# Kernel tuning notes

Measured on AMD Instinct MI355X. Metric: run time of the kernel, lower is better.

## Reference

```python
import jax, jax.numpy as jnp
import numpy as np

D_MODEL = 2048
NUM_HEADS = 16
HEAD_DIM = D_MODEL // NUM_HEADS  # 128


def setup_inputs() -> dict:
    key = jax.random.key(0)
    ks = jax.random.split(key, 9)
    s = 0.02
    x = jax.random.normal(ks[0], (2, 2048, D_MODEL), dtype=jnp.float32)
    Wq = jax.random.normal(ks[1], (D_MODEL, D_MODEL), dtype=jnp.float32) * s
    bq = jnp.zeros((D_MODEL,), dtype=jnp.float32)
    Wk = jax.random.normal(ks[2], (D_MODEL, HEAD_DIM), dtype=jnp.float32) * s
    bk = jnp.zeros((HEAD_DIM,), dtype=jnp.float32)
    Wv = jax.random.normal(ks[3], (D_MODEL, HEAD_DIM), dtype=jnp.float32) * s
    bv = jnp.zeros((HEAD_DIM,), dtype=jnp.float32)
    Wo = jax.random.normal(ks[4], (D_MODEL, D_MODEL), dtype=jnp.float32) * s
    bo = jnp.zeros((D_MODEL,), dtype=jnp.float32)
    return {"x": x, "Wq": Wq, "bq": bq, "Wk": Wk, "bk": bk,
            "Wv": Wv, "bv": bv, "Wo": Wo, "bo": bo}


def reference(x, Wq, bq, Wk, bk, Wv, bv, Wo, bo):
    B, S, _ = x.shape
    # projections
    q = (x @ Wq + bq).reshape(B, S, NUM_HEADS, HEAD_DIM)  # [B,S,H,d]
    k = x @ Wk + bk  # [B,S,d] shared across heads (MQA)
    v = x @ Wv + bv  # [B,S,d]
    scale = 1.0 / jnp.sqrt(jnp.float32(HEAD_DIM))
    # QK^T with shared K: [B,H,Sq,Sk]
    scores = jnp.einsum('bqhd,bkd->bhqk', q, k) * scale
    attn = jax.nn.softmax(scores, axis=-1)
    # AV with shared V: [B,H,Sq,d]
    out = jnp.einsum('bhqk,bkd->bqhd', attn, v).reshape(B, S, D_MODEL)
    return out @ Wo + bo
```

## Files before the change

kernel.cpp:

```cpp
#include <hip/hip_runtime.h>


typedef __attribute__((ext_vector_type(8))) short short8;
typedef __attribute__((ext_vector_type(4))) float f32x4;
typedef __attribute__((ext_vector_type(4))) unsigned int uint4v;

__device__ __forceinline__ unsigned short f2bf(float f) {
  unsigned int u = __float_as_uint(f);
  u += 0x7FFF + ((u >> 16) & 1);
  return (unsigned short)(u >> 16);
}

__device__ __forceinline__ unsigned int pk2(float a, float b) {
  return (unsigned int)f2bf(a) | ((unsigned int)f2bf(b) << 16);
}

__device__ __forceinline__ void gll16(const void* g, void* lds) {
  __builtin_amdgcn_global_load_lds(
      (const __attribute__((address_space(1))) unsigned int*)g,
      (__attribute__((address_space(3))) unsigned int*)lds, 16, 0, 0);
}

__global__ __launch_bounds__(256) void cvtk(const float* __restrict__ in,
                                            unsigned short* __restrict__ out, int n4) {
  int i = blockIdx.x * blockDim.x + threadIdx.x;
  int stride = gridDim.x * blockDim.x;
  for (; i < n4; i += stride) {
    float4 v = reinterpret_cast<const float4*>(in)[i];
    ushort4 o;
    o.x = f2bf(v.x); o.y = f2bf(v.y); o.z = f2bf(v.z); o.w = f2bf(v.w);
    reinterpret_cast<ushort4*>(out)[i] = o;
  }
}

__global__ __launch_bounds__(256) void tcvt2(const float* __restrict__ W0, const float* __restrict__ W1,
                                             unsigned short* __restrict__ D0, unsigned short* __restrict__ D1,
                                             int K, int N) {
  const float* W = blockIdx.z ? W1 : W0;
  unsigned short* Wt = blockIdx.z ? D1 : D0;
  __shared__ float tile[32][33];
  int n0 = blockIdx.x * 32, k0 = blockIdx.y * 32;
  int tx = threadIdx.x, ty = threadIdx.y;
  #pragma unroll
  for (int i = 0; i < 32; i += 8)
    tile[ty + i][tx] = W[(size_t)(k0 + ty + i) * N + n0 + tx];
  __syncthreads();
  #pragma unroll
  for (int i = 0; i < 32; i += 8)
    Wt[(size_t)(n0 + ty + i) * K + k0 + tx] = f2bf(tile[tx][ty + i]);
}

template <int MODE>
__global__ __launch_bounds__(256)
void gemm_nt(const unsigned short* __restrict__ A, const unsigned short* __restrict__ Bt,
             const float* __restrict__ b0, const float* __restrict__ b1,
             const float* __restrict__ b2,
             void* __restrict__ C, unsigned short* __restrict__ C2,
             unsigned short* __restrict__ C3, int M, int N, int K, float cmul) {
  __shared__ unsigned short lA[128 * 64];
  __shared__ unsigned short lB[128 * 64];
  const int t = threadIdx.x;
  const int lane = t & 63;
  const int w = t >> 6;
  const int wr = w >> 1, wc = w & 1;
  const int r15 = lane & 15, g4 = lane >> 4;
  const int tileM = blockIdx.y * 128;
  const int tileN = blockIdx.x * 128;

  f32x4 acc[4][4];
  #pragma unroll
  for (int i = 0; i < 4; i++)
    #pragma unroll
    for (int j = 0; j < 4; j++) acc[i][j] = (f32x4){0.f, 0.f, 0.f, 0.f};

  const int nkt = K >> 6;
  for (int kt = 0; kt < nkt; ++kt) {
    const int k0 = kt * 64;
    #pragma unroll
    for (int i = 0; i < 4; ++i) {
      int flat = i * 256 + t;
      int row = flat >> 3, gc = flat & 7;
      unsigned lb = (unsigned)(i * 256 + w * 64) * 16;
      gll16(A  + (size_t)(tileM + row) * K + k0 + gc * 8, (char*)lA + lb);
      gll16(Bt + (size_t)(tileN + row) * K + k0 + gc * 8, (char*)lB + lb);
    }
    __syncthreads();
    #pragma unroll
    for (int kk = 0; kk < 2; ++kk) {
      short8 af[4], bf[4];
      #pragma unroll
      for (int mt = 0; mt < 4; ++mt)
        af[mt] = *reinterpret_cast<const short8*>(&lA[(wr * 64 + mt * 16 + r15) * 64 + kk * 32 + g4 * 8]);
      #pragma unroll
      for (int nt = 0; nt < 4; ++nt)
        bf[nt] = *reinterpret_cast<const short8*>(&lB[(wc * 64 + nt * 16 + r15) * 64 + kk * 32 + g4 * 8]);
      #pragma unroll
      for (int mt = 0; mt < 4; ++mt)
        #pragma unroll
        for (int nt = 0; nt < 4; ++nt)
          acc[mt][nt] = __builtin_amdgcn_mfma_f32_16x16x32_bf16(af[mt], bf[nt], acc[mt][nt], 0, 0, 0);
    }
    __syncthreads();
  }

  #pragma unroll
  for (int mt = 0; mt < 4; ++mt) {
    #pragma unroll
    for (int nt = 0; nt < 4; ++nt) {
      int col = tileN + wc * 64 + nt * 16 + r15;
      #pragma unroll
      for (int r = 0; r < 4; ++r) {
        int row = tileM + wr * 64 + mt * 16 + g4 * 4 + r;
        float v = acc[mt][nt][r];
        if (MODE == 1) {
          ((float*)C)[(size_t)row * N + col] = v + b0[col];
        } else {
          if (col < 2048) {
            ((unsigned short*)C)[(size_t)row * 2048 + col] = f2bf((v + b0[col]) * cmul);
          } else if (col < 2176) {
            int dd = col - 2048;
            C2[(size_t)row * 128 + dd] = f2bf(v + b1[dd]);
          } else {
            int dd = col - 2176;
            int bb = row >> 11, s = row & 2047;
            C3[((size_t)bb * 128 + dd) * 2048 + s] = f2bf(v + b2[dd]);
          }
        }
      }
    }
  }
}

__global__ __launch_bounds__(256)
void flash_mqa(const unsigned short* __restrict__ qb, const unsigned short* __restrict__ kb,
               const unsigned short* __restrict__ vt, unsigned short* __restrict__ ob) {
  __shared__ unsigned short lK[2][64 * 128];
  __shared__ unsigned short lV[2][128 * 64];
  __shared__ unsigned short lP[4][16 * 64];

  const int t = threadIdx.x;
  const int lane = t & 63;
  const int w = t >> 6;
  const int r15 = lane & 15, g4 = lane >> 4;
  const int qt = blockIdx.x, h = blockIdx.y, b = blockIdx.z;
  const int q0 = qt * 64 + w * 16;

  short8 qf[4];
  const size_t qrow = (size_t)(b * 2048 + q0 + r15);
  #pragma unroll
  for (int kk = 0; kk < 4; ++kk)
    qf[kk] = *reinterpret_cast<const short8*>(&qb[qrow * 2048 + h * 128 + kk * 32 + g4 * 8]);

  f32x4 oacc[8];
  #pragma unroll
  for (int i = 0; i < 8; i++) oacc[i] = (f32x4){0.f, 0.f, 0.f, 0.f};
  float m_q = -1e30f, l_q = 0.f;

  const unsigned short* kbase = kb + (size_t)b * 2048 * 128;
  const unsigned short* vbase = vt + (size_t)b * 128 * 2048;

  auto stage = [&](int buf, int kv0) {
    #pragma unroll
    for (int i = 0; i < 4; ++i) {
      int flat = i * 256 + t;
      unsigned lb = (unsigned)(i * 256 + w * 64) * 16;
      { int row = flat >> 4, gc = flat & 15;
        gll16(kbase + (size_t)(kv0 + row) * 128 + ((gc ^ (row & 15)) << 3), (char*)lK[buf] + lb); }
      { int row = flat >> 3, gc = flat & 7;
        gll16(vbase + (size_t)row * 2048 + kv0 + ((gc ^ (row & 7)) << 3), (char*)lV[buf] + lb); }
    }
  };

  stage(0, 0);
  int cur = 0;
  for (int it = 0; it < 32; ++it) {
    if (it < 31) {
      stage(cur ^ 1, (it + 1) * 64);
      asm volatile("s_waitcnt vmcnt(8)" ::: "memory");
    } else {
      asm volatile("s_waitcnt vmcnt(0)" ::: "memory");
    }
    __builtin_amdgcn_s_barrier();
    asm volatile("" ::: "memory");

    const unsigned short* cK = lK[cur];
    const unsigned short* cV = lV[cur];

    f32x4 s[4];
    #pragma unroll
    for (int ct = 0; ct < 4; ct++) s[ct] = (f32x4){0.f, 0.f, 0.f, 0.f};
    #pragma unroll
    for (int kk = 0; kk < 4; ++kk) {
      #pragma unroll
      for (int ct = 0; ct < 4; ++ct) {
        const int krow = ct * 16 + r15;
        const int kg = (kk * 4 + g4) ^ (krow & 15);
        short8 kf = *reinterpret_cast<const short8*>(&cK[krow * 128 + kg * 8]);
        s[ct] = __builtin_amdgcn_mfma_f32_16x16x32_bf16(kf, qf[kk], s[ct], 0, 0, 0);
      }
    }

    float mx = s[0][0];
    #pragma unroll
    for (int ct = 0; ct < 4; ++ct)
      #pragma unroll
      for (int r = 0; r < 4; ++r) mx = fmaxf(mx, s[ct][r]);
    mx = fmaxf(mx, __shfl_xor(mx, 16));
    mx = fmaxf(mx, __shfl_xor(mx, 32));
    if (__any(mx > m_q + 8.f)) {
      float mn = fmaxf(m_q, mx);
      float rf = __expf(m_q - mn);
      m_q = mn;
      l_q *= rf;
      #pragma unroll
      for (int ot = 0; ot < 8; ++ot)
        #pragma unroll
        for (int r = 0; r < 4; ++r) oacc[ot][r] *= rf;
    }
    #pragma unroll
    for (int ct = 0; ct < 4; ++ct) {
      float p0 = __expf(s[ct][0] - m_q);
      float p1 = __expf(s[ct][1] - m_q);
      float p2 = __expf(s[ct][2] - m_q);
      float p3 = __expf(s[ct][3] - m_q);
      l_q += (p0 + p1) + (p2 + p3);
      const int gi = (ct * 4 + g4) ^ r15;
      *reinterpret_cast<uint2*>(&lP[w][r15 * 64 + gi * 4]) = make_uint2(pk2(p0, p1), pk2(p2, p3));
    }

    #pragma unroll
    for (int kk = 0; kk < 2; ++kk) {
      const int gA = (kk * 8 + g4 * 2) ^ r15;
      const int gB = (kk * 8 + g4 * 2 + 1) ^ r15;
      const uint2 wa = *reinterpret_cast<const uint2*>(&lP[w][r15 * 64 + gA * 4]);
      const uint2 wb = *reinterpret_cast<const uint2*>(&lP[w][r15 * 64 + gB * 4]);
      uint4v pw = {wa.x, wa.y, wb.x, wb.y};
      short8 pf = __builtin_bit_cast(short8, pw);
      #pragma unroll
      for (int ot = 0; ot < 8; ++ot) {
        const int vrow = ot * 16 + r15;
        const int vg = (kk * 4 + g4) ^ (vrow & 7);
        short8 vf = *reinterpret_cast<const short8*>(&cV[vrow * 64 + vg * 8]);
        oacc[ot] = __builtin_amdgcn_mfma_f32_16x16x32_bf16(vf, pf, oacc[ot], 0, 0, 0);
      }
    }

    asm volatile("" ::: "memory");
    __builtin_amdgcn_s_barrier();
    cur ^= 1;
  }

  float l = l_q;
  l += __shfl_xor(l, 16);
  l += __shfl_xor(l, 32);
  const float inv = 1.0f / l;
  const int row = q0 + r15;
  const size_t base = ((size_t)(b * 2048 + row)) * 2048 + h * 128;
  #pragma unroll
  for (int ot = 0; ot < 8; ++ot) {
    uint2 pw = make_uint2(pk2(oacc[ot][0] * inv, oacc[ot][1] * inv),
                          pk2(oacc[ot][2] * inv, oacc[ot][3] * inv));
    *reinterpret_cast<uint2*>(&ob[base + ot * 16 + g4 * 4]) = pw;
  }
}

extern "C" void kernel_launch(void* const* d_in, const int* in_sizes, int n_in,
                              void* d_out, int out_size, void* d_ws, size_t ws_size,
                              hipStream_t stream) {
  const float* x  = (const float*)d_in[0];
  const float* Wq = (const float*)d_in[1];
  const float* bq = (const float*)d_in[2];
  const float* Wk = (const float*)d_in[3];
  const float* bk = (const float*)d_in[4];
  const float* Wv = (const float*)d_in[5];
  const float* bv = (const float*)d_in[6];
  const float* Wo = (const float*)d_in[7];
  const float* bo = (const float*)d_in[8];
  float* out = (float*)d_out;

  char* ws = (char*)d_ws;
  size_t off = 0;
  auto alloc = [&](size_t elems) {
    unsigned short* p = (unsigned short*)(ws + off);
    off += (elems * 2 + 255) & ~(size_t)255;
    return p;
  };
  unsigned short* xb    = alloc(8388608);
  unsigned short* qb    = alloc(8388608);
  unsigned short* ob    = alloc(8388608);
  unsigned short* wqkvt = alloc(4718592);
  unsigned short* wot   = alloc(4194304);
  unsigned short* kbuf  = alloc(524288);
  unsigned short* vtb   = alloc(524288);

  const float scale = 0.08838834764831845f;

  dim3 tb(32, 8);
  cvtk<<<4096, 256, 0, stream>>>(x, xb, 2097152);
  tcvt2<<<dim3(64, 64, 2), tb, 0, stream>>>(Wq, Wo, wqkvt, wot, 2048, 2048);
  tcvt2<<<dim3(4, 64, 2),  tb, 0, stream>>>(Wk, Wv, wqkvt + (size_t)2048 * 2048,
                                            wqkvt + (size_t)2176 * 2048, 2048, 128);

  gemm_nt<3><<<dim3(18, 32), 256, 0, stream>>>(xb, wqkvt, bq, bk, bv,
                                               qb, kbuf, vtb, 4096, 2304, 2048, scale);
  flash_mqa<<<dim3(32, 16, 2), 256, 0, stream>>>(qb, kbuf, vtb, ob);
  gemm_nt<1><<<dim3(16, 32), 256, 0, stream>>>(ob, wot, bo, nullptr, nullptr,
                                               out, nullptr, nullptr, 4096, 2048, 2048, 1.0f);
}
```

Before: 289.9 us.

## Process two heads per flash block to reuse staged K/V; use exp2 softmax

Each flash-attention block now handles two query heads against the shared MQA K/V tiles, so every K/V tile staged into LDS is reused twice. This halves the grid and the global-to-LDS traffic per head. Separately, log2(e) is folded into the Q scale so the softmax can use exp2f, with the rescale threshold adjusted to match. The block holds twice the accumulators and Q fragments in registers, which may lower occupancy, and with half as many blocks the GPU may be less evenly filled.

```diff
diff --git a/kernel.cpp b/kernel.cpp
--- a/kernel.cpp
+++ b/kernel.cpp
@@ -142,19 +142,24 @@
   const int lane = t & 63;
   const int w = t >> 6;
   const int r15 = lane & 15, g4 = lane >> 4;
-  const int qt = blockIdx.x, h = blockIdx.y, b = blockIdx.z;
+  const int qt = blockIdx.x, hy = blockIdx.y, b = blockIdx.z;
   const int q0 = qt * 64 + w * 16;
 
-  short8 qf[4];
+  short8 qf[2][4];
   const size_t qrow = (size_t)(b * 2048 + q0 + r15);
   #pragma unroll
-  for (int kk = 0; kk < 4; ++kk)
-    qf[kk] = *reinterpret_cast<const short8*>(&qb[qrow * 2048 + h * 128 + kk * 32 + g4 * 8]);
-
-  f32x4 oacc[8];
-  #pragma unroll
-  for (int i = 0; i < 8; i++) oacc[i] = (f32x4){0.f, 0.f, 0.f, 0.f};
-  float m_q = -1e30f, l_q = 0.f;
+  for (int hh = 0; hh < 2; ++hh)
+    #pragma unroll
+    for (int kk = 0; kk < 4; ++kk)
+      qf[hh][kk] = *reinterpret_cast<const short8*>(
+          &qb[qrow * 2048 + (hy * 2 + hh) * 128 + kk * 32 + g4 * 8]);
+
+  f32x4 oacc[2][8];
+  #pragma unroll
+  for (int hh = 0; hh < 2; ++hh)
+    #pragma unroll
+    for (int i = 0; i < 8; i++) oacc[hh][i] = (f32x4){0.f, 0.f, 0.f, 0.f};
+  float m_q[2] = {-1e30f, -1e30f}, l_q[2] = {0.f, 0.f};
 
   const unsigned short* kbase = kb + (size_t)b * 2048 * 128;
   const unsigned short* vbase = vt + (size_t)b * 128 * 2048;
@@ -186,62 +191,65 @@
     const unsigned short* cK = lK[cur];
     const unsigned short* cV = lV[cur];
 
-    f32x4 s[4];
-    #pragma unroll
-    for (int ct = 0; ct < 4; ct++) s[ct] = (f32x4){0.f, 0.f, 0.f, 0.f};
-    #pragma unroll
-    for (int kk = 0; kk < 4; ++kk) {
+    #pragma unroll
+    for (int hh = 0; hh < 2; ++hh) {
+      f32x4 s[4];
+      #pragma unroll
+      for (int ct = 0; ct < 4; ct++) s[ct] = (f32x4){0.f, 0.f, 0.f, 0.f};
+      #pragma unroll
+      for (int kk = 0; kk < 4; ++kk) {
+        #pragma unroll
+        for (int ct = 0; ct < 4; ++ct) {
+          const int krow = ct * 16 + r15;
+          const int kg = (kk * 4 + g4) ^ (krow & 15);
+          short8 kf = *reinterpret_cast<const short8*>(&cK[krow * 128 + kg * 8]);
+          s[ct] = __builtin_amdgcn_mfma_f32_16x16x32_bf16(kf, qf[hh][kk], s[ct], 0, 0, 0);
+        }
+      }
+
+      float mx = s[0][0];
+      #pragma unroll
+      for (int ct = 0; ct < 4; ++ct)
+        #pragma unroll
+        for (int r = 0; r < 4; ++r) mx = fmaxf(mx, s[ct][r]);
+      mx = fmaxf(mx, __shfl_xor(mx, 16));
+      mx = fmaxf(mx, __shfl_xor(mx, 32));
+      if (__any(mx > m_q[hh] + 11.5416f)) {
+        float mn = fmaxf(m_q[hh], mx);
+        float rf = exp2f(m_q[hh] - mn);
+        m_q[hh] = mn;
+        l_q[hh] *= rf;
+        #pragma unroll
+        for (int ot = 0; ot < 8; ++ot)
+          #pragma unroll
+          for (int r = 0; r < 4; ++r) oacc[hh][ot][r] *= rf;
+      }
       #pragma unroll
       for (int ct = 0; ct < 4; ++ct) {
-        const int krow = ct * 16 + r15;
-        const int kg = (kk * 4 + g4) ^ (krow & 15);
-        short8 kf = *reinterpret_cast<const short8*>(&cK[krow * 128 + kg * 8]);
-        s[ct] = __builtin_amdgcn_mfma_f32_16x16x32_bf16(kf, qf[kk], s[ct], 0, 0, 0);
-      }
-    }
-
-    float mx = s[0][0];
-    #pragma unroll
-    for (int ct = 0; ct < 4; ++ct)
-      #pragma unroll
-      for (int r = 0; r < 4; ++r) mx = fmaxf(mx, s[ct][r]);
-    mx = fmaxf(mx, __shfl_xor(mx, 16));
-    mx = fmaxf(mx, __shfl_xor(mx, 32));
-    if (__any(mx > m_q + 8.f)) {
-      float mn = fmaxf(m_q, mx);
-      float rf = __expf(m_q - mn);
-      m_q = mn;
-      l_q *= rf;
-      #pragma unroll
-      for (int ot = 0; ot < 8; ++ot)
-        #pragma unroll
-        for (int r = 0; r < 4; ++r) oacc[ot][r] *= rf;
-    }
-    #pragma unroll
-    for (int ct = 0; ct < 4; ++ct) {
-      float p0 = __expf(s[ct][0] - m_q);
-      float p1 = __expf(s[ct][1] - m_q);
-      float p2 = __expf(s[ct][2] - m_q);
-      float p3 = __expf(s[ct][3] - m_q);
-      l_q += (p0 + p1) + (p2 + p3);
-      const int gi = (ct * 4 + g4) ^ r15;
-      *reinterpret_cast<uint2*>(&lP[w][r15 * 64 + gi * 4]) = make_uint2(pk2(p0, p1), pk2(p2, p3));
-    }
-
-    #pragma unroll
-    for (int kk = 0; kk < 2; ++kk) {
-      const int gA = (kk * 8 + g4 * 2) ^ r15;
-      const int gB = (kk * 8 + g4 * 2 + 1) ^ r15;
-      const uint2 wa = *reinterpret_cast<const uint2*>(&lP[w][r15 * 64 + gA * 4]);
-      const uint2 wb = *reinterpret_cast<const uint2*>(&lP[w][r15 * 64 + gB * 4]);
-      uint4v pw = {wa.x, wa.y, wb.x, wb.y};
-      short8 pf = __builtin_bit_cast(short8, pw);
-      #pragma unroll
-      for (int ot = 0; ot < 8; ++ot) {
-        const int vrow = ot * 16 + r15;
-        const int vg = (kk * 4 + g4) ^ (vrow & 7);
-        short8 vf = *reinterpret_cast<const short8*>(&cV[vrow * 64 + vg * 8]);
-        oacc[ot] = __builtin_amdgcn_mfma_f32_16x16x32_bf16(vf, pf, oacc[ot], 0, 0, 0);
+        float p0 = exp2f(s[ct][0] - m_q[hh]);
+        float p1 = exp2f(s[ct][1] - m_q[hh]);
+        float p2 = exp2f(s[ct][2] - m_q[hh]);
+        float p3 = exp2f(s[ct][3] - m_q[hh]);
+        l_q[hh] += (p0 + p1) + (p2 + p3);
+        const int gi = (ct * 4 + g4) ^ r15;
+        *reinterpret_cast<uint2*>(&lP[w][r15 * 64 + gi * 4]) = make_uint2(pk2(p0, p1), pk2(p2, p3));
+      }
+
+      #pragma unroll
+      for (int kk = 0; kk < 2; ++kk) {
+        const int gA = (kk * 8 + g4 * 2) ^ r15;
+        const int gB = (kk * 8 + g4 * 2 + 1) ^ r15;
+        const uint2 wa = *reinterpret_cast<const uint2*>(&lP[w][r15 * 64 + gA * 4]);
+        const uint2 wb = *reinterpret_cast<const uint2*>(&lP[w][r15 * 64 + gB * 4]);
+        uint4v pw = {wa.x, wa.y, wb.x, wb.y};
+        short8 pf = __builtin_bit_cast(short8, pw);
+        #pragma unroll
+        for (int ot = 0; ot < 8; ++ot) {
+          const int vrow = ot * 16 + r15;
+          const int vg = (kk * 4 + g4) ^ (vrow & 7);
+          short8 vf = *reinterpret_cast<const short8*>(&cV[vrow * 64 + vg * 8]);
+          oacc[hh][ot] = __builtin_amdgcn_mfma_f32_16x16x32_bf16(vf, pf, oacc[hh][ot], 0, 0, 0);
+        }
       }
     }
 
@@ -250,17 +258,20 @@
     cur ^= 1;
   }
 
-  float l = l_q;
-  l += __shfl_xor(l, 16);
-  l += __shfl_xor(l, 32);
-  const float inv = 1.0f / l;
-  const int row = q0 + r15;
-  const size_t base = ((size_t)(b * 2048 + row)) * 2048 + h * 128;
-  #pragma unroll
-  for (int ot = 0; ot < 8; ++ot) {
-    uint2 pw = make_uint2(pk2(oacc[ot][0] * inv, oacc[ot][1] * inv),
-                          pk2(oacc[ot][2] * inv, oacc[ot][3] * inv));
-    *reinterpret_cast<uint2*>(&ob[base + ot * 16 + g4 * 4]) = pw;
+  #pragma unroll
+  for (int hh = 0; hh < 2; ++hh) {
+    float l = l_q[hh];
+    l += __shfl_xor(l, 16);
+    l += __shfl_xor(l, 32);
+    const float inv = 1.0f / l;
+    const int row = q0 + r15;
+    const size_t base = ((size_t)(b * 2048 + row)) * 2048 + (hy * 2 + hh) * 128;
+    #pragma unroll
+    for (int ot = 0; ot < 8; ++ot) {
+      uint2 pw = make_uint2(pk2(oacc[hh][ot][0] * inv, oacc[hh][ot][1] * inv),
+                            pk2(oacc[hh][ot][2] * inv, oacc[hh][ot][3] * inv));
+      *reinterpret_cast<uint2*>(&ob[base + ot * 16 + g4 * 4]) = pw;
+    }
   }
 }
 
@@ -293,7 +304,7 @@
   unsigned short* kbuf  = alloc(524288);
   unsigned short* vtb   = alloc(524288);
 
-  const float scale = 0.08838834764831845f;
+  const float qscale = 0.08838834764831845f * 1.44269504088896f;
 
   dim3 tb(32, 8);
   cvtk<<<4096, 256, 0, stream>>>(x, xb, 2097152);
@@ -302,8 +313,8 @@
                                             wqkvt + (size_t)2176 * 2048, 2048, 128);
 
   gemm_nt<3><<<dim3(18, 32), 256, 0, stream>>>(xb, wqkvt, bq, bk, bv,
-                                               qb, kbuf, vtb, 4096, 2304, 2048, scale);
-  flash_mqa<<<dim3(32, 16, 2), 256, 0, stream>>>(qb, kbuf, vtb, ob);
+                                               qb, kbuf, vtb, 4096, 2304, 2048, qscale);
+  flash_mqa<<<dim3(32, 8, 2), 256, 0, stream>>>(qb, kbuf, vtb, ob);
   gemm_nt<1><<<dim3(16, 32), 256, 0, stream>>>(ob, wot, bo, nullptr, nullptr,
                                                out, nullptr, nullptr, 4096, 2048, 2048, 1.0f);
 }
```

Result: no change. 287.0 us (-1.0%).
